# Kernel optimization log

Measured on AMD Instinct MI355X. Metric: run time of the kernel, lower is better.

The kernel has to match this reference:

```python
import jax, jax.numpy as jnp
import numpy as np

N = 100000          # active voxels
KS = 7              # kernel size per spatial dim
K = KS ** 3         # 343 kernel offsets
G = 64              # voxel grid extent
INPLANES = 128
PLANES = 128
D2 = PLANES // 4    # 32
EPS = 1e-5


def _build_neighbor_map(seed=0):
    # Random distinct voxel coordinates in a G^3 grid, then for every point and
    # every 7^3 offset find the index of the neighboring voxel (-1 if absent).
    rng = np.random.default_rng(seed)
    lin = rng.choice(G ** 3, size=N, replace=False)
    coords = np.stack(np.unravel_index(lin, (G, G, G)), axis=1).astype(np.int64)  # [N,3]
    keys = coords[:, 0] * G * G + coords[:, 1] * G + coords[:, 2]
    order = np.argsort(keys)
    skeys = keys[order]
    offs = np.arange(KS) - KS // 2
    off_grid = np.stack(np.meshgrid(offs, offs, offs, indexing='ij'), axis=-1).reshape(K, 3)
    q = coords[:, None, :] + off_grid[None, :, :]          # [N,K,3]
    inb = np.all((q >= 0) & (q < G), axis=-1)
    qk = q[..., 0] * G * G + q[..., 1] * G + q[..., 2]
    pos = np.searchsorted(skeys, qk)
    pos_c = np.clip(pos, 0, N - 1)
    found = inb & (skeys[pos_c] == qk)
    nbr = np.where(found, order[pos_c], -1).astype(np.int32)  # [N,K]
    return jnp.asarray(nbr)


def setup_inputs() -> dict:
    key = jax.random.key(0)
    k = jax.random.split(key, 4)
    feats = jax.random.normal(k[0], (N, INPLANES), jnp.float32)
    w1 = jax.random.normal(k[1], (INPLANES, D2), jnp.float32) / np.sqrt(INPLANES)
    w_conv = jax.random.normal(k[2], (K, D2, D2), jnp.float32) / np.sqrt(K * D2)
    w2 = jax.random.normal(k[3], (D2, PLANES), jnp.float32) / np.sqrt(D2)
    return {
        'feats': feats,
        'nbr': _build_neighbor_map(),
        'w1': w1,
        'ln1_g': jnp.ones((D2,), jnp.float32),
        'ln1_b': jnp.zeros((D2,), jnp.float32),
        'w_conv': w_conv,
        'w2': w2,
        'ln2_g': jnp.ones((PLANES,), jnp.float32),
        'ln2_b': jnp.zeros((PLANES,), jnp.float32),
    }


def _layernorm(x, g, b):
    m = jnp.mean(x, axis=-1, keepdims=True)
    v = jnp.var(x, axis=-1, keepdims=True)
    return (x - m) * jax.lax.rsqrt(v + EPS) * g + b


def _sparse_conv(x, nbr, w):
    # x: [N,d2], nbr: [N,K], w: [K,d2,d2]; gather-apply-scatter per kernel offset.
    def step(acc, inp):
        idx, wk = inp                                # idx: [N], wk: [d2,d2]
        valid = (idx >= 0).astype(x.dtype)[:, None]
        g = jnp.take(x, jnp.maximum(idx, 0), axis=0) * valid
        return acc + g @ wk, None
    acc0 = jnp.zeros((x.shape[0], w.shape[2]), x.dtype)
    out, _ = jax.lax.scan(step, acc0, (nbr.T, w))
    return out


def reference(feats, nbr, w1, ln1_g, ln1_b, w_conv, w2, ln2_g, ln2_b):
    shortcut = feats                                  # inplanes == planes -> Identity
    h = _layernorm(feats @ w1, ln1_g, ln1_b)          # unary_1: [N,d2]
    h = _sparse_conv(h, nbr, w_conv)                  # 7^3 sparse conv: [N,d2]
    h = _layernorm(h @ w2, ln2_g, ln2_b)              # unary_2: [N,planes]
    h = jax.nn.gelu(h, approximate=False)             # drop_path is Identity (rate 0)
    return h + shortcut
```

## Files before the change

### kernel.cpp

```cpp
#include <hip/hip_runtime.h>
#include <hip/hip_bf16.h>

#define N_PTS 100000
#define KOFF 343
#define EPS 1e-5f

typedef __hip_bfloat16 bf16;
typedef __attribute__((ext_vector_type(4))) float f32x4;
typedef __attribute__((ext_vector_type(16))) float f32x16;
typedef __attribute__((ext_vector_type(8))) short s16x8;

__global__ __launch_bounds__(256) void pack_kernel(const float* __restrict__ w_conv,
                                                   bf16* __restrict__ wpk) {
  int t = blockIdx.x * 256 + threadIdx.x;
  if (t >= KOFF * 128) return;
  int l = t & 63;
  int s = (t >> 6) & 1;
  int k = t >> 7;
  int col = l & 31;
  int kq = l >> 5;
  const float* wk = w_conv + k * 1024;
  s16x8 v;
  for (int j = 0; j < 8; ++j) {
    bf16 h = __float2bfloat16(wk[(s * 16 + kq * 8 + j) * 32 + col]);
    short sv;
    __builtin_memcpy(&sv, &h, 2);
    v[j] = sv;
  }
  *reinterpret_cast<s16x8*>(reinterpret_cast<char*>(wpk) + (size_t)t * 16) = v;
}

__global__ __launch_bounds__(256) void unary1_kernel(const float* __restrict__ feats,
    const float* __restrict__ w1, const float* __restrict__ g1,
    const float* __restrict__ b1, bf16* __restrict__ h1b) {
  __shared__ float sf[8][128];
  __shared__ float sw[128 * 32];
  int tid = threadIdx.x;
  int rbase = blockIdx.x * 8;
  for (int i = tid; i < 1024; i += 256)
    reinterpret_cast<f32x4*>(sw)[i] = reinterpret_cast<const f32x4*>(w1)[i];
  {
    int i = tid;
    int r = rbase + (i >> 5);
    f32x4 v = reinterpret_cast<const f32x4*>(feats)[(size_t)r * 32 + (i & 31)];
    reinterpret_cast<f32x4*>(&sf[0][0])[i] = v;
  }
  __syncthreads();
  int half = tid >> 5;
  int c = tid & 31;
  int r = rbase + half;
  const float* frow = sf[half];
  float acc = 0.f;
  #pragma unroll 8
  for (int kk = 0; kk < 128; ++kk)
    acc += frow[kk] * sw[kk * 32 + c];
  float s = acc, s2 = acc * acc;
  #pragma unroll
  for (int m = 16; m >= 1; m >>= 1) {
    s  += __shfl_xor(s,  m, 64);
    s2 += __shfl_xor(s2, m, 64);
  }
  float mean = s * (1.f / 32.f);
  float var  = s2 * (1.f / 32.f) - mean * mean;
  float y = (acc - mean) * rsqrtf(var + EPS) * g1[c] + b1[c];
  h1b[(size_t)r * 32 + c] = __float2bfloat16(y);
}

__global__ __launch_bounds__(256) void conv_kernel(const bf16* __restrict__ h1b,
    const int* __restrict__ nbr, const bf16* __restrict__ wpk,
    float* __restrict__ h2) {
  __shared__ int snbr[32 * 345];
  int tid = threadIdx.x;
  int wave = tid >> 6;
  int l = tid & 63;
  int col = l & 31;
  int kq = l >> 5;
  int pbase = blockIdx.x * 32;
  {
    const int* g = nbr + (size_t)pbase * KOFF;
    for (int i = tid; i < 32 * KOFF; i += 256) {
      unsigned row = (unsigned)i / KOFF;
      unsigned kk = (unsigned)i - row * KOFF;
      snbr[row * 345 + kk] = g[i];
    }
  }
  __syncthreads();
  int k0 = (KOFF * wave) >> 2;
  int k1 = (KOFF * (wave + 1)) >> 2;
  f32x16 acc;
  #pragma unroll
  for (int i = 0; i < 16; ++i) acc[i] = 0.f;
  const s16x8* wb = reinterpret_cast<const s16x8*>(wpk);
  const s16x8 zv = {0, 0, 0, 0, 0, 0, 0, 0};
  const int* myrow = snbr + col * 345;
  for (int kb = k0; kb < k1; kb += 4) {
    int id[4];
    s16x8 A0[4], A1[4], B0[4], B1[4];
    #pragma unroll
    for (int j = 0; j < 4; ++j) {
      int k = kb + j;
      id[j] = (k < k1) ? myrow[k] : -1;
    }
    #pragma unroll
    for (int j = 0; j < 4; ++j) {
      int k = kb + j;
      int kc = (k < k1) ? k : (k1 - 1);
      const s16x8* r = reinterpret_cast<const s16x8*>(h1b + (size_t)(id[j] < 0 ? 0 : id[j]) * 32);
      A0[j] = r[kq];
      A1[j] = r[2 + kq];
      B0[j] = wb[(size_t)kc * 128 + l];
      B1[j] = wb[(size_t)kc * 128 + 64 + l];
    }
    #pragma unroll
    for (int j = 0; j < 4; ++j) {
      s16x8 a0 = id[j] < 0 ? zv : A0[j];
      s16x8 a1 = id[j] < 0 ? zv : A1[j];
      acc = __builtin_amdgcn_mfma_f32_32x32x16_bf16(a0, B0[j], acc, 0, 0, 0);
      acc = __builtin_amdgcn_mfma_f32_32x32x16_bf16(a1, B1[j], acc, 0, 0, 0);
    }
  }
  __syncthreads();
  float* red = reinterpret_cast<float*>(snbr);
  #pragma unroll
  for (int reg = 0; reg < 16; ++reg) {
    int rrow = (reg & 3) + 8 * (reg >> 2) + 4 * kq;
    red[wave * 1024 + rrow * 32 + col] = acc[reg];
  }
  __syncthreads();
  const f32x4* rv = reinterpret_cast<const f32x4*>(red);
  f32x4 s = rv[tid] + rv[256 + tid] + rv[512 + tid] + rv[768 + tid];
  reinterpret_cast<f32x4*>(h2 + (size_t)pbase * 32)[tid] = s;
}

__global__ __launch_bounds__(256) void unary2_kernel(const float* __restrict__ h2,
    const float* __restrict__ w2, const float* __restrict__ g2,
    const float* __restrict__ b2, const float* __restrict__ feats,
    float* __restrict__ out) {
  int tid = threadIdx.x;
  int wave = tid >> 6;
  int l = tid & 63;
  int r = blockIdx.x * 4 + wave;
  const float* hrow = h2 + (size_t)r * 32;
  float acc0 = 0.f, acc1 = 0.f;
  #pragma unroll
  for (int q = 0; q < 8; ++q) {
    f32x4 hv = reinterpret_cast<const f32x4*>(hrow)[q];
    #pragma unroll
    for (int j = 0; j < 4; ++j) {
      int kk = q * 4 + j;
      float h = hv[j];
      acc0 += h * w2[kk * 128 + l];
      acc1 += h * w2[kk * 128 + 64 + l];
    }
  }
  float s = acc0 + acc1, s2 = acc0 * acc0 + acc1 * acc1;
  #pragma unroll
  for (int m = 32; m >= 1; m >>= 1) {
    s  += __shfl_xor(s,  m, 64);
    s2 += __shfl_xor(s2, m, 64);
  }
  float mean = s * (1.f / 128.f);
  float var  = s2 * (1.f / 128.f) - mean * mean;
  float inv = rsqrtf(var + EPS);
  float y0 = (acc0 - mean) * inv * g2[l] + b2[l];
  float y1 = (acc1 - mean) * inv * g2[64 + l] + b2[64 + l];
  float ge0 = 0.5f * y0 * (1.f + erff(y0 * 0.70710678118f));
  float ge1 = 0.5f * y1 * (1.f + erff(y1 * 0.70710678118f));
  out[(size_t)r * 128 + l]      = ge0 + feats[(size_t)r * 128 + l];
  out[(size_t)r * 128 + 64 + l] = ge1 + feats[(size_t)r * 128 + 64 + l];
}

extern "C" void kernel_launch(void* const* d_in, const int* in_sizes, int n_in,
                              void* d_out, int out_size, void* d_ws, size_t ws_size,
                              hipStream_t stream) {
  const float* feats  = (const float*)d_in[0];
  const int*   nbr    = (const int*)d_in[1];
  const float* w1     = (const float*)d_in[2];
  const float* ln1_g  = (const float*)d_in[3];
  const float* ln1_b  = (const float*)d_in[4];
  const float* w_conv = (const float*)d_in[5];
  const float* w2     = (const float*)d_in[6];
  const float* ln2_g  = (const float*)d_in[7];
  const float* ln2_b  = (const float*)d_in[8];
  float* out = (float*)d_out;
  char* ws = (char*)d_ws;
  bf16*  h1b = (bf16*)ws;
  bf16*  wpk = (bf16*)(ws + 6400000);
  float* h2  = (float*)(ws + 7102464);

  hipLaunchKernelGGL(pack_kernel,   dim3((KOFF * 128 + 255) / 256), dim3(256), 0, stream, w_conv, wpk);
  hipLaunchKernelGGL(unary1_kernel, dim3(N_PTS / 8),                dim3(256), 0, stream, feats, w1, ln1_g, ln1_b, h1b);
  hipLaunchKernelGGL(conv_kernel,   dim3(N_PTS / 32),               dim3(256), 0, stream, h1b, nbr, wpk, h2);
  hipLaunchKernelGGL(unary2_kernel, dim3(N_PTS / 4),                dim3(256), 0, stream, h2, w2, ln2_g, ln2_b, feats, out);
}
```

Before: 328.5 us.

## Stage neighbor map in two halves to halve LDS; process two rows per wave in unary2

The conv kernel now loads the neighbor map into shared memory in two rounds of about 172 offsets each, roughly halving its LDS footprint (~44KB to ~22KB) so more blocks can be resident per CU for latency hiding. The cost is an extra load phase and barriers between rounds, and waves sit idle while each half is loaded. Separately, unary2 has each wave handle two rows so the w2 loads are reused across rows, and it launches half as many blocks.

```diff
diff --git a/kernel.cpp b/kernel.cpp
--- a/kernel.cpp
+++ b/kernel.cpp
@@ -4,6 +4,8 @@
 #define N_PTS 100000
 #define KOFF 343
 #define EPS 1e-5f
+#define NTILES 3125
+#define SSTR 173
 
 typedef __hip_bfloat16 bf16;
 typedef __attribute__((ext_vector_type(4))) float f32x4;
@@ -66,61 +68,76 @@
   h1b[(size_t)r * 32 + c] = __float2bfloat16(y);
 }
 
-__global__ __launch_bounds__(256) void conv_kernel(const bf16* __restrict__ h1b,
+template<int KCNT, int KBASE>
+__device__ __forceinline__ void process_round(const int* __restrict__ snbr,
+    const bf16* __restrict__ h1b, const s16x8* __restrict__ wb,
+    f32x16& acc, int wave, int l, int col, int kq) {
+  int k0 = (KCNT * wave) >> 2;
+  int k1 = (KCNT * (wave + 1)) >> 2;
+  const int* myrow = snbr + col * SSTR;
+  const s16x8 zv = {0, 0, 0, 0, 0, 0, 0, 0};
+  for (int kb = k0; kb < k1; kb += 4) {
+    int id[4];
+    s16x8 A0[4], A1[4], B0[4], B1[4];
+    #pragma unroll
+    for (int j = 0; j < 4; ++j) {
+      int k = kb + j;
+      id[j] = (k < k1) ? myrow[k] : -1;
+    }
+    #pragma unroll
+    for (int j = 0; j < 4; ++j) {
+      int k = kb + j;
+      int kc = (k < k1) ? k : (k1 - 1);
+      const s16x8* r = reinterpret_cast<const s16x8*>(h1b + (size_t)(id[j] < 0 ? 0 : id[j]) * 32);
+      A0[j] = r[kq];
+      A1[j] = r[2 + kq];
+      B0[j] = wb[(size_t)(KBASE + kc) * 128 + l];
+      B1[j] = wb[(size_t)(KBASE + kc) * 128 + 64 + l];
+    }
+    #pragma unroll
+    for (int j = 0; j < 4; ++j) {
+      s16x8 a0 = id[j] < 0 ? zv : A0[j];
+      s16x8 a1 = id[j] < 0 ? zv : A1[j];
+      acc = __builtin_amdgcn_mfma_f32_32x32x16_bf16(a0, B0[j], acc, 0, 0, 0);
+      acc = __builtin_amdgcn_mfma_f32_32x32x16_bf16(a1, B1[j], acc, 0, 0, 0);
+    }
+  }
+}
+
+__global__ __launch_bounds__(256) void conv_r2_kernel(const bf16* __restrict__ h1b,
     const int* __restrict__ nbr, const bf16* __restrict__ wpk,
     float* __restrict__ h2) {
-  __shared__ int snbr[32 * 345];
+  __shared__ int sbuf[32 * SSTR];
   int tid = threadIdx.x;
   int wave = tid >> 6;
   int l = tid & 63;
   int col = l & 31;
   int kq = l >> 5;
   int pbase = blockIdx.x * 32;
-  {
-    const int* g = nbr + (size_t)pbase * KOFF;
-    for (int i = tid; i < 32 * KOFF; i += 256) {
-      unsigned row = (unsigned)i / KOFF;
-      unsigned kk = (unsigned)i - row * KOFF;
-      snbr[row * 345 + kk] = g[i];
-    }
-  }
-  __syncthreads();
-  int k0 = (KOFF * wave) >> 2;
-  int k1 = (KOFF * (wave + 1)) >> 2;
+  const int* g = nbr + (size_t)pbase * KOFF;
+  const s16x8* wb = reinterpret_cast<const s16x8*>(wpk);
   f32x16 acc;
   #pragma unroll
   for (int i = 0; i < 16; ++i) acc[i] = 0.f;
-  const s16x8* wb = reinterpret_cast<const s16x8*>(wpk);
-  const s16x8 zv = {0, 0, 0, 0, 0, 0, 0, 0};
-  const int* myrow = snbr + col * 345;
-  for (int kb = k0; kb < k1; kb += 4) {
-    int id[4];
-    s16x8 A0[4], A1[4], B0[4], B1[4];
-    #pragma unroll
-    for (int j = 0; j < 4; ++j) {
-      int k = kb + j;
-      id[j] = (k < k1) ? myrow[k] : -1;
-    }
-    #pragma unroll
-    for (int j = 0; j < 4; ++j) {
-      int k = kb + j;
-      int kc = (k < k1) ? k : (k1 - 1);
-      const s16x8* r = reinterpret_cast<const s16x8*>(h1b + (size_t)(id[j] < 0 ? 0 : id[j]) * 32);
-      A0[j] = r[kq];
-      A1[j] = r[2 + kq];
-      B0[j] = wb[(size_t)kc * 128 + l];
-      B1[j] = wb[(size_t)kc * 128 + 64 + l];
-    }
-    #pragma unroll
-    for (int j = 0; j < 4; ++j) {
-      s16x8 a0 = id[j] < 0 ? zv : A0[j];
-      s16x8 a1 = id[j] < 0 ? zv : A1[j];
-      acc = __builtin_amdgcn_mfma_f32_32x32x16_bf16(a0, B0[j], acc, 0, 0, 0);
-      acc = __builtin_amdgcn_mfma_f32_32x32x16_bf16(a1, B1[j], acc, 0, 0, 0);
-    }
-  }
-  __syncthreads();
-  float* red = reinterpret_cast<float*>(snbr);
+
+  for (int i = tid; i < 32 * 172; i += 256) {
+    int row = i / 172;
+    int kk = i - row * 172;
+    sbuf[row * SSTR + kk] = g[row * KOFF + kk];
+  }
+  __syncthreads();
+  process_round<172, 0>(sbuf, h1b, wb, acc, wave, l, col, kq);
+  __syncthreads();
+  for (int i = tid; i < 32 * 171; i += 256) {
+    int row = i / 171;
+    int kk = i - row * 171;
+    sbuf[row * SSTR + kk] = g[row * KOFF + 172 + kk];
+  }
+  __syncthreads();
+  process_round<171, 172>(sbuf, h1b, wb, acc, wave, l, col, kq);
+  __syncthreads();
+
+  float* red = reinterpret_cast<float*>(sbuf);
   #pragma unroll
   for (int reg = 0; reg < 16; ++reg) {
     int rrow = (reg & 3) + 8 * (reg >> 2) + 4 * kq;
@@ -139,35 +156,52 @@
   int tid = threadIdx.x;
   int wave = tid >> 6;
   int l = tid & 63;
-  int r = blockIdx.x * 4 + wave;
-  const float* hrow = h2 + (size_t)r * 32;
-  float acc0 = 0.f, acc1 = 0.f;
+  int r0 = blockIdx.x * 8 + wave * 2;
+  const f32x4* h0 = reinterpret_cast<const f32x4*>(h2 + (size_t)r0 * 32);
+  const f32x4* h1r = reinterpret_cast<const f32x4*>(h2 + (size_t)(r0 + 1) * 32);
+  float a00 = 0.f, a01 = 0.f, a10 = 0.f, a11 = 0.f;
   #pragma unroll
   for (int q = 0; q < 8; ++q) {
-    f32x4 hv = reinterpret_cast<const f32x4*>(hrow)[q];
+    f32x4 v0 = h0[q];
+    f32x4 v1 = h1r[q];
     #pragma unroll
     for (int j = 0; j < 4; ++j) {
       int kk = q * 4 + j;
-      float h = hv[j];
-      acc0 += h * w2[kk * 128 + l];
-      acc1 += h * w2[kk * 128 + 64 + l];
-    }
-  }
-  float s = acc0 + acc1, s2 = acc0 * acc0 + acc1 * acc1;
+      float wlo = w2[kk * 128 + l];
+      float whi = w2[kk * 128 + 64 + l];
+      a00 += v0[j] * wlo;  a01 += v0[j] * whi;
+      a10 += v1[j] * wlo;  a11 += v1[j] * whi;
+    }
+  }
+  float s0 = a00 + a01, q0 = a00 * a00 + a01 * a01;
+  float s1 = a10 + a11, q1 = a10 * a10 + a11 * a11;
   #pragma unroll
   for (int m = 32; m >= 1; m >>= 1) {
-    s  += __shfl_xor(s,  m, 64);
-    s2 += __shfl_xor(s2, m, 64);
-  }
-  float mean = s * (1.f / 128.f);
-  float var  = s2 * (1.f / 128.f) - mean * mean;
-  float inv = rsqrtf(var + EPS);
-  float y0 = (acc0 - mean) * inv * g2[l] + b2[l];
-  float y1 = (acc1 - mean) * inv * g2[64 + l] + b2[64 + l];
-  float ge0 = 0.5f * y0 * (1.f + erff(y0 * 0.70710678118f));
-  float ge1 = 0.5f * y1 * (1.f + erff(y1 * 0.70710678118f));
-  out[(size_t)r * 128 + l]      = ge0 + feats[(size_t)r * 128 + l];
-  out[(size_t)r * 128 + 64 + l] = ge1 + feats[(size_t)r * 128 + 64 + l];
+    s0 += __shfl_xor(s0, m, 64);
+    q0 += __shfl_xor(q0, m, 64);
+    s1 += __shfl_xor(s1, m, 64);
+    q1 += __shfl_xor(q1, m, 64);
+  }
+  float m0 = s0 * (1.f / 128.f);
+  float v0 = q0 * (1.f / 128.f) - m0 * m0;
+  float i0 = rsqrtf(v0 + EPS);
+  float m1 = s1 * (1.f / 128.f);
+  float v1 = q1 * (1.f / 128.f) - m1 * m1;
+  float i1 = rsqrtf(v1 + EPS);
+  float glo = g2[l], ghi = g2[64 + l];
+  float blo = b2[l], bhi = b2[64 + l];
+  float y00 = (a00 - m0) * i0 * glo + blo;
+  float y01 = (a01 - m0) * i0 * ghi + bhi;
+  float y10 = (a10 - m1) * i1 * glo + blo;
+  float y11 = (a11 - m1) * i1 * ghi + bhi;
+  float e00 = 0.5f * y00 * (1.f + erff(y00 * 0.70710678118f));
+  float e01 = 0.5f * y01 * (1.f + erff(y01 * 0.70710678118f));
+  float e10 = 0.5f * y10 * (1.f + erff(y10 * 0.70710678118f));
+  float e11 = 0.5f * y11 * (1.f + erff(y11 * 0.70710678118f));
+  out[(size_t)r0 * 128 + l]            = e00 + feats[(size_t)r0 * 128 + l];
+  out[(size_t)r0 * 128 + 64 + l]       = e01 + feats[(size_t)r0 * 128 + 64 + l];
+  out[(size_t)(r0 + 1) * 128 + l]      = e10 + feats[(size_t)(r0 + 1) * 128 + l];
+  out[(size_t)(r0 + 1) * 128 + 64 + l] = e11 + feats[(size_t)(r0 + 1) * 128 + 64 + l];
 }
 
 extern "C" void kernel_launch(void* const* d_in, const int* in_sizes, int n_in,
@@ -188,8 +222,8 @@
   bf16*  wpk = (bf16*)(ws + 6400000);
   float* h2  = (float*)(ws + 7102464);
 
-  hipLaunchKernelGGL(pack_kernel,   dim3((KOFF * 128 + 255) / 256), dim3(256), 0, stream, w_conv, wpk);
-  hipLaunchKernelGGL(unary1_kernel, dim3(N_PTS / 8),                dim3(256), 0, stream, feats, w1, ln1_g, ln1_b, h1b);
-  hipLaunchKernelGGL(conv_kernel,   dim3(N_PTS / 32),               dim3(256), 0, stream, h1b, nbr, wpk, h2);
-  hipLaunchKernelGGL(unary2_kernel, dim3(N_PTS / 4),                dim3(256), 0, stream, h2, w2, ln2_g, ln2_b, feats, out);
-}
+  hipLaunchKernelGGL(pack_kernel,    dim3((KOFF * 128 + 255) / 256), dim3(256), 0, stream, w_conv, wpk);
+  hipLaunchKernelGGL(unary1_kernel,  dim3(N_PTS / 8),                dim3(256), 0, stream, feats, w1, ln1_g, ln1_b, h1b);
+  hipLaunchKernelGGL(conv_r2_kernel, dim3(NTILES),                   dim3(256), 0, stream, h1b, nbr, wpk, h2);
+  hipLaunchKernelGGL(unary2_kernel,  dim3(N_PTS / 8),                dim3(256), 0, stream, h2, w2, ln2_g, ln2_b, feats, out);
+}
```

After: 309.4 us, median of 2. -5.8%, faster.
